# Optimization experiments

Hardware: AMD Instinct MI355X
Metric: run time of the kernel (lower is better)

## Reference

```python
import jax, jax.numpy as jnp
import numpy as np

QMIN, QMAX = -128.0, 127.0


def setup_inputs() -> dict:
    key = jax.random.key(0)
    k1, k2, k3, k4, k5 = jax.random.split(key, 5)
    B, S, IN, OUT = 4, 2048, 4096, 11008
    hidden_states = jax.random.normal(k1, (B, S, IN), dtype=jnp.float16)
    # symmetric per-channel int8 weights (stored as int32 for harness compat)
    weight = jax.random.randint(k2, (OUT, IN), -128, 128, dtype=jnp.int32)
    weight_scale = jax.random.uniform(k3, (OUT,), dtype=jnp.float32, minval=0.001, maxval=0.02)
    input_scale = jax.random.uniform(k4, (1,), dtype=jnp.float32, minval=0.01, maxval=0.05)
    pre_quant_scale = jax.random.uniform(k5, (IN,), dtype=jnp.float32, minval=0.5, maxval=1.5).astype(jnp.float16)
    return {
        "hidden_states": hidden_states,
        "weight": weight,
        "weight_scale": weight_scale,
        "input_scale": input_scale,
        "pre_quant_scale": pre_quant_scale,
    }


def reference(hidden_states, weight, weight_scale, input_scale, pre_quant_scale):
    # SmoothQuant smoothing (fp16 elementwise Mul)
    x_smooth = hidden_states * pre_quant_scale  # [B,S,IN] fp16
    # Per-tensor activation fake-quant (Q + DQ), done in fp32 like QuantizeLinear
    s = input_scale.astype(jnp.float32)  # [1]
    q = jnp.clip(jnp.round(x_smooth.astype(jnp.float32) / s), QMIN, QMAX)
    x_dq = (q * s).astype(jnp.float16)  # [B,S,IN]
    # Per-channel weight dequant (axis=0 -> out_features)
    w_dq = (weight.astype(jnp.float32) * weight_scale[:, None]).astype(jnp.float16)  # [OUT,IN]
    # F.linear: x @ W^T  (emulated int8 GEMM in fp16)
    return jnp.einsum('bsi,oi->bso', x_dq, w_dq)
```

## Files before the change

### kernel.cpp

```cpp
#include <hip/hip_runtime.h>
#include <hip/hip_fp16.h>
#include <stdint.h>

typedef int i32x4 __attribute__((ext_vector_type(4)));

#define IN_F  4096
#define OUT_F 11008
#define MROWS 8192
#define BM 256
#define BN 256
#define BKB 64
#define NKT (IN_F / BKB)
#define GRID_M (MROWS / BM)
#define GRID_N (OUT_F / BN)
#define NBLK (GRID_M * GRID_N)

#define AS1 __attribute__((address_space(1)))
#define AS3 __attribute__((address_space(3)))

__global__ __launch_bounds__(256) void quant_act_kernel(
    const float* __restrict__ x, const float* __restrict__ pqs,
    const float* __restrict__ iscale, int8_t* __restrict__ q)
{
    const int i = blockIdx.x * blockDim.x + threadIdx.x;
    const float s = iscale[0];
    const size_t base = (size_t)i * 8;
    const int col = (int)(base & (IN_F - 1));

    const float4 x0 = *(const float4*)(x + base);
    const float4 x1 = *(const float4*)(x + base + 4);
    const float4 p0 = *(const float4*)(pqs + col);
    const float4 p1 = *(const float4*)(pqs + col + 4);

    float xs[8];
    xs[0] = x0.x * p0.x; xs[1] = x0.y * p0.y; xs[2] = x0.z * p0.z; xs[3] = x0.w * p0.w;
    xs[4] = x1.x * p1.x; xs[5] = x1.y * p1.y; xs[6] = x1.z * p1.z; xs[7] = x1.w * p1.w;

    unsigned int lo = 0, hi = 0;
    #pragma unroll
    for (int j = 0; j < 8; ++j) {
        float xm = __half2float(__float2half(xs[j]));
        float qf = nearbyintf(xm / s);
        qf = fminf(fmaxf(qf, -128.0f), 127.0f);
        unsigned int b = (unsigned int)((int)qf & 0xff);
        if (j < 4) lo |= b << (8 * j);
        else       hi |= b << (8 * (j - 4));
    }
    *(uint2*)(q + base) = make_uint2(lo, hi);
}

__global__ __launch_bounds__(256) void pack_w_kernel(
    const int* __restrict__ w, int8_t* __restrict__ wq)
{
    const size_t i = (size_t)(blockIdx.x * blockDim.x + threadIdx.x) * 8;
    const int4 a = *(const int4*)(w + i);
    const int4 b = *(const int4*)(w + i + 4);
    unsigned int lo = (a.x & 0xff) | ((a.y & 0xff) << 8) | ((a.z & 0xff) << 16) | ((unsigned int)(a.w & 0xff) << 24);
    unsigned int hi = (b.x & 0xff) | ((b.y & 0xff) << 8) | ((b.z & 0xff) << 16) | ((unsigned int)(b.w & 0xff) << 24);
    *(uint2*)(wq + i) = make_uint2(lo, hi);
}

__global__ __launch_bounds__(512, 2) void gemm_i8_256_kernel(
    const int8_t* __restrict__ Aq,
    const int8_t* __restrict__ Wq,
    const float* __restrict__ wscale,
    const float* __restrict__ iscale,
    float* __restrict__ out)
{
    __shared__ int8_t lds[98304];

    const int tid  = threadIdx.x;
    const int lane = tid & 63;
    const int wv   = tid >> 6;
    const int wr   = wv >> 2;
    const int wc   = wv & 3;

    const int bid = (int)blockIdx.x;
    const int swz = (bid & 7) * (NBLK / 8) + (bid >> 3);
    const int bm = swz / GRID_N;
    const int bn = swz % GRID_N;
    const int brow = bm * BM, bcol = bn * BN;

    const int8_t* Ab = Aq + (size_t)brow * IN_F;
    const int8_t* Bb = Wq + (size_t)bcol * IN_F;

    int srow[2], scol[2], sdst[2];
    #pragma unroll
    for (int i = 0; i < 2; ++i) {
        const int n = i * 512 + tid;
        srow[i] = n >> 2;
        scol[i] = ((n & 3) ^ ((srow[i] >> 1) & 3)) * 16;
        sdst[i] = n * 16;
    }

    #define STAGE_A(t) do { AS3 int8_t* Ad = (AS3 int8_t*)(lds + ((t) % 3) * 32768); \
        const int k0_ = (t) * BKB; \
        _Pragma("unroll") for (int i_ = 0; i_ < 2; ++i_) \
            __builtin_amdgcn_global_load_lds((const AS1 void*)(Ab + (size_t)srow[i_] * IN_F + k0_ + scol[i_]), \
                                             (AS3 void*)(Ad + sdst[i_]), 16, 0, 0); } while (0)
    #define STAGE_B(t) do { AS3 int8_t* Bd = (AS3 int8_t*)(lds + ((t) % 3) * 32768 + 16384); \
        const int k0_ = (t) * BKB; \
        _Pragma("unroll") for (int i_ = 0; i_ < 2; ++i_) \
            __builtin_amdgcn_global_load_lds((const AS1 void*)(Bb + (size_t)srow[i_] * IN_F + k0_ + scol[i_]), \
                                             (AS3 void*)(Bd + sdst[i_]), 16, 0, 0); } while (0)

    i32x4 acc[8][4] = {};

    const int rl = lane & 15;
    const int hk = lane >> 4;
    const int koff = ((hk ^ ((rl >> 1) & 3)) * 16);
    const int a_base = (wr * 128 + rl) * 64;
    const int b_base = (wc * 64 + rl) * 64;

    STAGE_A(0); STAGE_B(0);
    STAGE_A(1); STAGE_B(1);

    for (int kt = 0; kt < NKT; ++kt) {
        if (kt + 1 < NKT) asm volatile("s_waitcnt vmcnt(4)" ::: "memory");
        else              asm volatile("s_waitcnt vmcnt(0)" ::: "memory");
        __builtin_amdgcn_s_barrier();
        __builtin_amdgcn_sched_barrier(0);

        const int8_t* At = lds + (kt % 3) * 32768;
        const int8_t* Bt = At + 16384;

        i32x4 a0[4], b[4], a1[4];
        #pragma unroll
        for (int mf = 0; mf < 4; ++mf)
            a0[mf] = *(const i32x4*)(At + a_base + mf * 1024 + koff);
        #pragma unroll
        for (int nf = 0; nf < 4; ++nf)
            b[nf] = *(const i32x4*)(Bt + b_base + nf * 1024 + koff);
        if (kt + 2 < NKT) STAGE_A(kt + 2);
        __builtin_amdgcn_s_setprio(1);
        #pragma unroll
        for (int mf = 0; mf < 4; ++mf)
            #pragma unroll
            for (int nf = 0; nf < 4; ++nf)
                acc[mf][nf] = __builtin_amdgcn_mfma_i32_16x16x64_i8(a0[mf], b[nf], acc[mf][nf], 0, 0, 0);
        __builtin_amdgcn_s_setprio(0);
        __builtin_amdgcn_s_barrier();

        #pragma unroll
        for (int mf = 0; mf < 4; ++mf)
            a1[mf] = *(const i32x4*)(At + a_base + (mf + 4) * 1024 + koff);
        if (kt + 2 < NKT) STAGE_B(kt + 2);
        __builtin_amdgcn_s_setprio(1);
        #pragma unroll
        for (int mf = 0; mf < 4; ++mf)
            #pragma unroll
            for (int nf = 0; nf < 4; ++nf)
                acc[mf + 4][nf] = __builtin_amdgcn_mfma_i32_16x16x64_i8(a1[mf], b[nf], acc[mf + 4][nf], 0, 0, 0);
        __builtin_amdgcn_s_setprio(0);
    }

    const float s = iscale[0];
    #pragma unroll
    for (int nf = 0; nf < 4; ++nf) {
        const int col = bcol + wc * 64 + nf * 16 + rl;
        const float sc = s * wscale[col];
        #pragma unroll
        for (int mf = 0; mf < 8; ++mf) {
            const int r0 = brow + wr * 128 + mf * 16 + hk * 4;
            #pragma unroll
            for (int j = 0; j < 4; ++j)
                out[(size_t)(r0 + j) * OUT_F + col] = (float)acc[mf][nf][j] * sc;
        }
    }
    #undef STAGE_A
    #undef STAGE_B
}

__global__ __launch_bounds__(256) void simple_ref_kernel(
    const float* __restrict__ x, const int* __restrict__ w,
    const float* __restrict__ wsc, const float* __restrict__ isc,
    const float* __restrict__ pqs, float* __restrict__ out)
{
    const float s = isc[0];
    const int m = blockIdx.x;
    const int o = blockIdx.y * 256 + threadIdx.x;
    if (o >= OUT_F) return;
    const float wso = wsc[o];
    const float* xr = x + (size_t)m * IN_F;
    const int* wr = w + (size_t)o * IN_F;
    float acc = 0.0f;
    for (int k = 0; k < IN_F; ++k) {
        float xm = __half2float(__float2half(xr[k] * pqs[k]));
        float qf = nearbyintf(xm / s);
        qf = fminf(fmaxf(qf, -128.0f), 127.0f);
        float xdq = __half2float(__float2half(qf * s));
        float wdq = __half2float(__float2half((float)wr[k] * wso));
        acc = fmaf(xdq, wdq, acc);
    }
    out[(size_t)m * OUT_F + o] = acc;
}

extern "C" void kernel_launch(void* const* d_in, const int* in_sizes, int n_in,
                              void* d_out, int out_size, void* d_ws, size_t ws_size,
                              hipStream_t stream)
{
    const float* x   = nullptr;
    const int*   w   = nullptr;
    const float* wsc = nullptr;
    const float* isc = nullptr;
    const float* pqs = nullptr;
    for (int i = 0; i < n_in; ++i) {
        switch (in_sizes[i]) {
            case MROWS * IN_F:   x   = (const float*)d_in[i]; break;
            case OUT_F * IN_F:   w   = (const int*)d_in[i];   break;
            case OUT_F:          wsc = (const float*)d_in[i]; break;
            case 1:              isc = (const float*)d_in[i]; break;
            case IN_F:           pqs = (const float*)d_in[i]; break;
        }
    }
    float* out = (float*)d_out;

    const size_t need = (size_t)MROWS * IN_F + (size_t)OUT_F * IN_F;
    if (d_ws == nullptr || ws_size < need) {
        dim3 grid(MROWS, (OUT_F + 255) / 256);
        simple_ref_kernel<<<grid, 256, 0, stream>>>(x, w, wsc, isc, pqs, out);
        return;
    }

    int8_t* Aq = (int8_t*)d_ws;
    int8_t* Wq = Aq + (size_t)MROWS * IN_F;

    quant_act_kernel<<<(MROWS * IN_F / 8) / 256, 256, 0, stream>>>(x, pqs, isc, Aq);
    pack_w_kernel<<<(OUT_F * IN_F / 8) / 256, 256, 0, stream>>>(w, Wq);
    gemm_i8_256_kernel<<<NBLK, 512, 0, stream>>>(Aq, Wq, wsc, isc, out);
}
```

Baseline: 494.5 us.

## Split GEMM block into 16 waves with 64x64 tiles and simpler pipeline

The int8 GEMM block grows from 512 to 1024 threads. Each of the 16 waves now computes a 64x64 sub-tile instead of 128x64, and each thread issues one A and one B async LDS load per stage. The two-phase loop with priority bumps and a mid-iteration barrier becomes a single phase that prefetches both operands up front. This lowers the accumulator count per wave and raises the number of waves available to hide latency, but each MFMA now needs more LDS reads. The launch bound of 1024 threads with 4 blocks per CU may also force a tight register cap and cause spills.

After: 484.2 us. 1.02x faster.

```diff
diff --git a/kernel.cpp b/kernel.cpp
--- a/kernel.cpp
+++ b/kernel.cpp
@@ -60,7 +60,7 @@
     *(uint2*)(wq + i) = make_uint2(lo, hi);
 }
 
-__global__ __launch_bounds__(512, 2) void gemm_i8_256_kernel(
+__global__ __launch_bounds__(1024, 4) void gemm_i8_256_kernel(
     const int8_t* __restrict__ Aq,
     const int8_t* __restrict__ Wq,
     const float* __restrict__ wscale,
@@ -84,74 +84,50 @@
     const int8_t* Ab = Aq + (size_t)brow * IN_F;
     const int8_t* Bb = Wq + (size_t)bcol * IN_F;
 
-    int srow[2], scol[2], sdst[2];
-    #pragma unroll
-    for (int i = 0; i < 2; ++i) {
-        const int n = i * 512 + tid;
-        srow[i] = n >> 2;
-        scol[i] = ((n & 3) ^ ((srow[i] >> 1) & 3)) * 16;
-        sdst[i] = n * 16;
-    }
-
-    #define STAGE_A(t) do { AS3 int8_t* Ad = (AS3 int8_t*)(lds + ((t) % 3) * 32768); \
-        const int k0_ = (t) * BKB; \
-        _Pragma("unroll") for (int i_ = 0; i_ < 2; ++i_) \
-            __builtin_amdgcn_global_load_lds((const AS1 void*)(Ab + (size_t)srow[i_] * IN_F + k0_ + scol[i_]), \
-                                             (AS3 void*)(Ad + sdst[i_]), 16, 0, 0); } while (0)
-    #define STAGE_B(t) do { AS3 int8_t* Bd = (AS3 int8_t*)(lds + ((t) % 3) * 32768 + 16384); \
-        const int k0_ = (t) * BKB; \
-        _Pragma("unroll") for (int i_ = 0; i_ < 2; ++i_) \
-            __builtin_amdgcn_global_load_lds((const AS1 void*)(Bb + (size_t)srow[i_] * IN_F + k0_ + scol[i_]), \
-                                             (AS3 void*)(Bd + sdst[i_]), 16, 0, 0); } while (0)
-
-    i32x4 acc[8][4] = {};
+    const int srow = tid >> 2;
+    const int scol = ((tid & 3) ^ ((srow >> 1) & 3)) * 16;
+    const int sdst = tid * 16;
+
+    #define STAGE_A(t) __builtin_amdgcn_global_load_lds( \
+        (const AS1 void*)(Ab + (size_t)srow * IN_F + (t) * BKB + scol), \
+        (AS3 void*)(lds + ((t) % 3) * 32768 + sdst), 16, 0, 0)
+    #define STAGE_B(t) __builtin_amdgcn_global_load_lds( \
+        (const AS1 void*)(Bb + (size_t)srow * IN_F + (t) * BKB + scol), \
+        (AS3 void*)(lds + ((t) % 3) * 32768 + 16384 + sdst), 16, 0, 0)
+
+    i32x4 acc[4][4] = {};
 
     const int rl = lane & 15;
     const int hk = lane >> 4;
-    const int koff = ((hk ^ ((rl >> 1) & 3)) * 16);
-    const int a_base = (wr * 128 + rl) * 64;
+    const int koff = (hk ^ ((rl >> 1) & 3)) * 16;
+    const int a_base = (wr * 64 + rl) * 64;
     const int b_base = (wc * 64 + rl) * 64;
 
     STAGE_A(0); STAGE_B(0);
     STAGE_A(1); STAGE_B(1);
 
     for (int kt = 0; kt < NKT; ++kt) {
-        if (kt + 1 < NKT) asm volatile("s_waitcnt vmcnt(4)" ::: "memory");
+        if (kt + 1 < NKT) asm volatile("s_waitcnt vmcnt(2)" ::: "memory");
         else              asm volatile("s_waitcnt vmcnt(0)" ::: "memory");
         __builtin_amdgcn_s_barrier();
-        __builtin_amdgcn_sched_barrier(0);
+
+        if (kt + 2 < NKT) { STAGE_A(kt + 2); STAGE_B(kt + 2); }
 
         const int8_t* At = lds + (kt % 3) * 32768;
         const int8_t* Bt = At + 16384;
 
-        i32x4 a0[4], b[4], a1[4];
+        i32x4 a[4], b[4];
         #pragma unroll
         for (int mf = 0; mf < 4; ++mf)
-            a0[mf] = *(const i32x4*)(At + a_base + mf * 1024 + koff);
+            a[mf] = *(const i32x4*)(At + a_base + mf * 1024 + koff);
         #pragma unroll
         for (int nf = 0; nf < 4; ++nf)
             b[nf] = *(const i32x4*)(Bt + b_base + nf * 1024 + koff);
-        if (kt + 2 < NKT) STAGE_A(kt + 2);
-        __builtin_amdgcn_s_setprio(1);
         #pragma unroll
         for (int mf = 0; mf < 4; ++mf)
             #pragma unroll
             for (int nf = 0; nf < 4; ++nf)
-                acc[mf][nf] = __builtin_amdgcn_mfma_i32_16x16x64_i8(a0[mf], b[nf], acc[mf][nf], 0, 0, 0);
-        __builtin_amdgcn_s_setprio(0);
-        __builtin_amdgcn_s_barrier();
-
-        #pragma unroll
-        for (int mf = 0; mf < 4; ++mf)
-            a1[mf] = *(const i32x4*)(At + a_base + (mf + 4) * 1024 + koff);
-        if (kt + 2 < NKT) STAGE_B(kt + 2);
-        __builtin_amdgcn_s_setprio(1);
-        #pragma unroll
-        for (int mf = 0; mf < 4; ++mf)
-            #pragma unroll
-            for (int nf = 0; nf < 4; ++nf)
-                acc[mf + 4][nf] = __builtin_amdgcn_mfma_i32_16x16x64_i8(a1[mf], b[nf], acc[mf + 4][nf], 0, 0, 0);
-        __builtin_amdgcn_s_setprio(0);
+                acc[mf][nf] = __builtin_amdgcn_mfma_i32_16x16x64_i8(a[mf], b[nf], acc[mf][nf], 0, 0, 0);
     }
 
     const float s = iscale[0];
@@ -160,8 +136,8 @@
         const int col = bcol + wc * 64 + nf * 16 + rl;
         const float sc = s * wscale[col];
         #pragma unroll
-        for (int mf = 0; mf < 8; ++mf) {
-            const int r0 = brow + wr * 128 + mf * 16 + hk * 4;
+        for (int mf = 0; mf < 4; ++mf) {
+            const int r0 = brow + wr * 64 + mf * 16 + hk * 4;
             #pragma unroll
             for (int j = 0; j < 4; ++j)
                 out[(size_t)(r0 + j) * OUT_F + col] = (float)acc[mf][nf][j] * sc;
@@ -227,5 +203,5 @@
 
     quant_act_kernel<<<(MROWS * IN_F / 8) / 256, 256, 0, stream>>>(x, pqs, isc, Aq);
     pack_w_kernel<<<(OUT_F * IN_F / 8) / 256, 256, 0, stream>>>(w, Wq);
-    gemm_i8_256_kernel<<<NBLK, 512, 0, stream>>>(Aq, Wq, wsc, isc, out);
-}
+    gemm_i8_256_kernel<<<NBLK, 1024, 0, stream>>>(Aq, Wq, wsc, isc, out);
+}
```
